# Performance work log

Measured on AMD Instinct MI355X. Metric: run time of the kernel, lower is better.

Reference implementation:

```python
import jax, jax.numpy as jnp
import numpy as np

N_NODES = 50000
N_EDGES = 800000
DIM = 128
HEADS = 4
NEG_SLOPE = 0.2
LN_EPS = 1e-5


def setup_inputs() -> dict:
    key = jax.random.key(0)
    ks = jax.random.split(key, 8)
    x = jax.random.normal(ks[0], (N_NODES, DIM), dtype=jnp.float32)
    edge_index = jax.random.randint(ks[1], (2, N_EDGES), 0, N_NODES, dtype=jnp.int32)
    W = jax.random.normal(ks[2], (DIM, DIM), dtype=jnp.float32) * (1.0 / np.sqrt(DIM))
    b = jnp.zeros((DIM,), dtype=jnp.float32)
    C = DIM // HEADS
    att_src = jax.random.normal(ks[3], (HEADS, C), dtype=jnp.float32) * 0.1
    att_dst = jax.random.normal(ks[4], (HEADS, C), dtype=jnp.float32) * 0.1
    ln_gamma = jnp.ones((DIM,), dtype=jnp.float32)
    ln_beta = jnp.zeros((DIM,), dtype=jnp.float32)
    prelu_w = jnp.full((1,), 0.25, dtype=jnp.float32)
    return {"x": x, "edge_index": edge_index, "W": W, "b": b,
            "att_src": att_src, "att_dst": att_dst,
            "ln_gamma": ln_gamma, "ln_beta": ln_beta, "prelu_w": prelu_w}


def reference(x, edge_index, W, b, att_src, att_dst, ln_gamma, ln_beta, prelu_w):
    N, D = x.shape
    H = HEADS
    C = D // H
    # shared linear transform (PyG GATConv lin_src == lin_dst for homogeneous input)
    xw = (x @ W).reshape(N, H, C)                      # [N,H,C]
    a_src = jnp.einsum('nhc,hc->nh', xw, att_src)      # [N,H]
    a_dst = jnp.einsum('nhc,hc->nh', xw, att_dst)      # [N,H]
    # add self loops (PyG default add_self_loops=True)
    loop = jnp.arange(N, dtype=edge_index.dtype)
    src = jnp.concatenate([edge_index[0], loop])       # [E+N]
    dst = jnp.concatenate([edge_index[1], loop])       # [E+N]
    # per-edge attention logits + segment softmax over destination
    alpha = jax.nn.leaky_relu(a_src[src] + a_dst[dst], NEG_SLOPE)   # [E+N,H]
    amax = jax.ops.segment_max(alpha, dst, num_segments=N)          # [N,H]
    alpha = jnp.exp(alpha - amax[dst])
    denom = jax.ops.segment_sum(alpha, dst, num_segments=N)         # [N,H]
    alpha = alpha / denom[dst]
    # weighted aggregation of source features
    msg = xw[src] * alpha[:, :, None]                               # [E+N,H,C]
    out = jax.ops.segment_sum(msg, dst, num_segments=N).reshape(N, D) + b
    # residual + LayerNorm + PReLU
    h = x + out
    mu = jnp.mean(h, axis=-1, keepdims=True)
    var = jnp.mean(jnp.square(h - mu), axis=-1, keepdims=True)
    h = (h - mu) * jax.lax.rsqrt(var + LN_EPS) * ln_gamma + ln_beta
    return jnp.where(h > 0, h, prelu_w[0] * h)
```

## Files before the change

### kernel.cpp

```cpp
#include <hip/hip_runtime.h>

#define NNODES 50000
#define NEDGES 800000
#define NEDGE4 200000
#define DIMF 128
#define NHEADS 4
#define NEG_SLOPE 0.2f
#define LN_EPS 1e-5f
#define SLOTS 64
#define NPERX 6250
#define NLB 782
#define SCB 2048

typedef int   v4i   __attribute__((ext_vector_type(4)));
typedef float v2f   __attribute__((ext_vector_type(2)));
typedef float v4f   __attribute__((ext_vector_type(4)));
typedef unsigned int v2u __attribute__((ext_vector_type(2)));
typedef short bf16x8 __attribute__((ext_vector_type(8)));
typedef float f32x4  __attribute__((ext_vector_type(4)));
typedef unsigned short u16x8 __attribute__((ext_vector_type(8)));

__device__ __forceinline__ unsigned short f2bf(float f) {
    unsigned int u = __float_as_uint(f);
    u = (u + 0x7fffu + ((u >> 16) & 1u)) >> 16;
    return (unsigned short)u;
}
__device__ __forceinline__ float bf2f(unsigned short u) {
    return __uint_as_float(((unsigned int)u) << 16);
}

__global__ __launch_bounds__(256) void k_prep(const float* __restrict__ W,
                                              unsigned short* __restrict__ WtG,
                                              int* __restrict__ cursor)
{
    const int idx = blockIdx.x * 256 + threadIdx.x;
    if (idx < DIMF * DIMF) {
        const int k = idx >> 7, col = idx & 127;
        WtG[col * 136 + k] = f2bf(W[idx]);
    }
    if (idx < NNODES) cursor[idx] = 0;
}

__global__ __launch_bounds__(256) void k_main(
    const float* __restrict__ x, const unsigned short* __restrict__ WtG,
    const float* __restrict__ att_src, const float* __restrict__ att_dst,
    unsigned char* __restrict__ xwb,
    float* __restrict__ asrc, float* __restrict__ adst,
    const int* __restrict__ esrc, const int* __restrict__ edst,
    int* __restrict__ cursor, unsigned short* __restrict__ perm)
{
    __shared__ unsigned short WtL[64 * 136];
    __shared__ float sAttS[128], sAttD[128];
    const int tid = threadIdx.x;

    if (blockIdx.x < SCB) {
        const int lo = (blockIdx.x & 7) * NPERX, hi = lo + NPERX;
        const v4i* es4 = (const v4i*)esrc;
        const v4i* ed4 = (const v4i*)edst;
        const int stride = (SCB >> 3) * 256;
        for (int e = (blockIdx.x >> 3) * 256 + tid; e < NEDGE4; e += stride) {
            v4i d4 = __builtin_nontemporal_load(ed4 + e);
            v4i s4 = __builtin_nontemporal_load(es4 + e);
            #pragma unroll
            for (int c = 0; c < 4; ++c) {
                const int dd = d4[c], ss = s4[c];
                if (dd >= lo && dd < hi) {
                    int p = atomicAdd(&cursor[dd], 1);
                    if (p < SLOTS) perm[(size_t)dd * SLOTS + p] = (unsigned short)ss;
                }
            }
        }
        return;
    }

    const int base = (blockIdx.x - SCB) * 64;

    if (tid < 128) sAttS[tid] = att_src[tid];
    else           sAttD[tid - 128] = att_dst[tid - 128];

    const int wv_   = tid >> 6;
    const int lane  = tid & 63;
    const int row16 = lane & 15;
    const int kg    = lane >> 4;
    const int grow_a = base + wv_ * 16 + row16;
    const int arow   = (grow_a < NNODES) ? grow_a : 0;

    bf16x8 af[4];
    #pragma unroll
    for (int ks = 0; ks < 4; ++ks) {
        const v4f* xr = (const v4f*)(x + (size_t)arow * DIMF + ks * 32 + kg * 8);
        const v4f xa = __builtin_nontemporal_load(xr);
        const v4f xb = __builtin_nontemporal_load(xr + 1);
        af[ks][0] = (short)f2bf(xa.x); af[ks][1] = (short)f2bf(xa.y);
        af[ks][2] = (short)f2bf(xa.z); af[ks][3] = (short)f2bf(xa.w);
        af[ks][4] = (short)f2bf(xb.x); af[ks][5] = (short)f2bf(xb.y);
        af[ks][6] = (short)f2bf(xb.z); af[ks][7] = (short)f2bf(xb.w);
    }

    f32x4 acc[8];
    #pragma unroll
    for (int ct = 0; ct < 8; ++ct) acc[ct] = (f32x4){0.f, 0.f, 0.f, 0.f};

    const uint4* g = (const uint4*)WtG;
    for (int hf = 0; hf < 2; ++hf) {
        __syncthreads();
        for (int i = tid; i < 1088; i += 256)
            ((uint4*)WtL)[i] = g[hf * 1088 + i];
        __syncthreads();
        #pragma unroll
        for (int ks = 0; ks < 4; ++ks) {
            #pragma unroll
            for (int ct = 0; ct < 4; ++ct) {
                const bf16x8 bfr = *(const bf16x8*)&WtL[(ct * 16 + row16) * 136 + ks * 32 + kg * 8];
                acc[hf * 4 + ct] = __builtin_amdgcn_mfma_f32_16x16x32_bf16(af[ks], bfr, acc[hf * 4 + ct], 0, 0, 0);
            }
        }
    }

    __syncthreads();
    unsigned short* OutL = WtL;
    #pragma unroll
    for (int ct = 0; ct < 8; ++ct) {
        #pragma unroll
        for (int r = 0; r < 4; ++r)
            OutL[(wv_ * 16 + kg * 4 + r) * 136 + ct * 16 + row16] = f2bf(acc[ct][r]);
    }
    __syncthreads();

    const int rowD = tid >> 2, seg = tid & 3;
    const int growD = base + rowD;
    if (growD < NNODES) {
        float ps = 0.f, pd = 0.f;
        #pragma unroll
        for (int q = 0; q < 4; ++q) {
            const u16x8 v = *(const u16x8*)&OutL[rowD * 136 + seg * 32 + q * 8];
            #pragma unroll
            for (int j = 0; j < 8; ++j) {
                const float f = bf2f(v[j]);
                const int c = seg * 32 + q * 8 + j;
                ps += f * sAttS[c];
                pd += f * sAttD[c];
            }
        }
        asrc[growD * NHEADS + seg] = ps;
        adst[growD * NHEADS + seg] = pd;
    }

    #pragma unroll
    for (int it = 0; it < 4; ++it) {
        const int f = tid + it * 256;
        const int row = f >> 4;
        const int c8  = (f & 15) * 8;
        if (base + row < NNODES) {
            const u16x8 v = *(const u16x8*)&OutL[row * 136 + c8];
            unsigned int lo, hi;
            lo = __builtin_amdgcn_cvt_pk_fp8_f32(bf2f(v[0]), bf2f(v[1]), 0, false);
            lo = __builtin_amdgcn_cvt_pk_fp8_f32(bf2f(v[2]), bf2f(v[3]), lo, true);
            hi = __builtin_amdgcn_cvt_pk_fp8_f32(bf2f(v[4]), bf2f(v[5]), 0, false);
            hi = __builtin_amdgcn_cvt_pk_fp8_f32(bf2f(v[6]), bf2f(v[7]), hi, true);
            v2u pk; pk.x = lo; pk.y = hi;
            __builtin_nontemporal_store(pk, (v2u*)(xwb + (size_t)(base + row) * DIMF + c8));
        }
    }
}

__global__ __launch_bounds__(256) void k_weights(
    const float4* __restrict__ asrc4, const float4* __restrict__ adst4,
    const int* __restrict__ cursor, const unsigned short* __restrict__ perm,
    ushort4* __restrict__ wperm)
{
    const int wid  = (blockIdx.x * 256 + threadIdx.x) >> 6;
    const int lane = threadIdx.x & 63;
    if (wid >= NNODES) return;

    int cnt = cursor[wid];
    if (cnt > SLOTS) cnt = SLOTS;
    const int cnt2 = (cnt + 15) & ~15;
    const float4 dv = adst4[wid];

    ushort4 wu = make_ushort4(0, 0, 0, 0);
    if (lane < cnt) {
        const int s = (int)perm[(size_t)wid * SLOTS + lane];
        const float4 ae = asrc4[s];
        float l0 = ae.x + dv.x, l1 = ae.y + dv.y;
        float l2 = ae.z + dv.z, l3 = ae.w + dv.w;
        l0 = (l0 > 0.f) ? l0 : NEG_SLOPE * l0;
        l1 = (l1 > 0.f) ? l1 : NEG_SLOPE * l1;
        l2 = (l2 > 0.f) ? l2 : NEG_SLOPE * l2;
        l3 = (l3 > 0.f) ? l3 : NEG_SLOPE * l3;
        wu.x = f2bf(__expf(l0)); wu.y = f2bf(__expf(l1));
        wu.z = f2bf(__expf(l2)); wu.w = f2bf(__expf(l3));
    }
    if (lane < cnt2) wperm[(size_t)wid * SLOTS + lane] = wu;
}

__global__ __launch_bounds__(256) void k_gat(
    const float* __restrict__ x, const float* __restrict__ bias,
    const float* __restrict__ asrc, const float* __restrict__ adst,
    const unsigned short* __restrict__ xwb16,
    const int* __restrict__ cursor, const unsigned short* __restrict__ perm,
    const unsigned short* __restrict__ wperm_u16,
    const float* __restrict__ ln_g, const float* __restrict__ ln_b,
    const float* __restrict__ prelu_w, float* __restrict__ out)
{
    const int wid  = (blockIdx.x * 256 + threadIdx.x) >> 6;
    const int lane = threadIdx.x & 63;
    if (wid >= NNODES) return;
    const int myh = lane >> 4;
    const int hb  = lane & 3;

    const float adh_b = adst[wid * NHEADS + hb];
    float lgS = asrc[wid * NHEADS + hb] + adh_b;
    lgS = (lgS > 0.f) ? lgS : NEG_SLOPE * lgS;
    const float wself_b = __expf(lgS);

    int cnt = cursor[wid];
    if (cnt > SLOTS) cnt = SLOTS;
    const int sidx = (lane < cnt) ? (int)perm[(size_t)wid * SLOTS + lane] : 0;

    const float wself = __shfl(wself_b, myh);
    const v2f pself = __builtin_amdgcn_cvt_pk_f32_fp8(
        (unsigned int)xwb16[(size_t)wid * 64 + lane], false);
    float acc0 = wself * pself.x;
    float acc1 = wself * pself.y;
    float dsum = 0.f;

    const int jmax = (cnt + 15) >> 4;
    for (int j = 0; j < jmax; ++j) {
        const unsigned short wu = wperm_u16[(size_t)wid * 256 + j * 64 + lane];
        const float wv = __uint_as_float(((unsigned)wu) << 16);
        dsum += wv;

        #pragma unroll
        for (int b = 0; b < 2; ++b) {
            const int ebase = j * 16 + b * 8;
            int s_[8]; float w_[8]; unsigned short v_[8];
            #pragma unroll
            for (int e = 0; e < 8; ++e) {
                s_[e] = __shfl(sidx, ebase + e);
                w_[e] = __shfl(wv, ((b * 8 + e) << 2) | myh);
            }
            #pragma unroll
            for (int e = 0; e < 8; ++e)
                v_[e] = xwb16[(size_t)s_[e] * 64 + lane];
            #pragma unroll
            for (int e = 0; e < 8; ++e) {
                const v2f p = __builtin_amdgcn_cvt_pk_f32_fp8((unsigned int)v_[e], false);
                acc0 += w_[e] * p.x;
                acc1 += w_[e] * p.y;
            }
        }
    }

    #pragma unroll
    for (int o = 4; o < 64; o <<= 1) dsum += __shfl_xor(dsum, o);
    const float wsum = __shfl(dsum + wself_b, myh);

    const float inv = 1.0f / wsum;
    const int c = lane * 2;
    const float2 xr = ((const float2*)x)[(size_t)wid * 64 + lane];
    float h0 = xr.x + acc0 * inv + bias[c];
    float h1 = xr.y + acc1 * inv + bias[c + 1];

    float s1 = h0 + h1, s2 = h0 * h0 + h1 * h1;
    #pragma unroll
    for (int o = 1; o < 64; o <<= 1) {
        s1 += __shfl_xor(s1, o);
        s2 += __shfl_xor(s2, o);
    }
    const float mu  = s1 * (1.f / 128.f);
    const float var = s2 * (1.f / 128.f) - mu * mu;
    const float r   = rsqrtf(var + LN_EPS);

    float g0 = (h0 - mu) * r * ln_g[c]     + ln_b[c];
    float g1 = (h1 - mu) * r * ln_g[c + 1] + ln_b[c + 1];
    const float pw = prelu_w[0];
    g0 = (g0 > 0.f) ? g0 : pw * g0;
    g1 = (g1 > 0.f) ? g1 : pw * g1;

    v2f gv; gv.x = g0; gv.y = g1;
    __builtin_nontemporal_store(gv, (v2f*)out + (size_t)wid * 64 + lane);
}

extern "C" void kernel_launch(void* const* d_in, const int* in_sizes, int n_in,
                              void* d_out, int out_size, void* d_ws, size_t ws_size,
                              hipStream_t stream)
{
    const float* x    = (const float*)d_in[0];
    const int*   eidx = (const int*)  d_in[1];
    const float* W    = (const float*)d_in[2];
    const float* bias = (const float*)d_in[3];
    const float* attS = (const float*)d_in[4];
    const float* attD = (const float*)d_in[5];
    const float* lng  = (const float*)d_in[6];
    const float* lnb  = (const float*)d_in[7];
    const float* pre  = (const float*)d_in[8];

    const int* esrc = eidx;
    const int* edst = eidx + NEDGES;

    unsigned char* xwb = (unsigned char*)d_ws;
    float* asrc    = (float*)(xwb + (size_t)NNODES * DIMF);
    float* adst    = asrc + (size_t)NNODES * NHEADS;
    int*   cursor  = (int*)(adst + (size_t)NNODES * NHEADS);
    unsigned short* perm = (unsigned short*)(cursor + NNODES);
    ushort4* wperm = (ushort4*)(perm + (size_t)NNODES * SLOTS);
    unsigned short* WtG = (unsigned short*)(wperm + (size_t)NNODES * SLOTS);

    k_prep<<<dim3(196), dim3(256), 0, stream>>>(W, WtG, cursor);

    k_main<<<dim3(SCB + NLB), dim3(256), 0, stream>>>(
        x, WtG, attS, attD, xwb, asrc, adst, esrc, edst, cursor, perm);

    k_weights<<<dim3((NNODES * 64 + 255) / 256), dim3(256), 0, stream>>>(
        (const float4*)asrc, (const float4*)adst, cursor, perm, wperm);

    k_gat<<<dim3((NNODES * 64 + 255) / 256), dim3(256), 0, stream>>>(
        x, bias, asrc, adst, (const unsigned short*)xwb, cursor, perm,
        (const unsigned short*)wperm, lng, lnb, pre, (float*)d_out);
}
```

Measured before the change: 107.4 us.

## Fuse attention weight computation into aggregation kernel and pack edge indices

Removes the separate k_weights kernel. Each wave now computes its node's per-edge exp attention weights directly and stages them in shared memory, which avoids a global write and re-read of the weight array and one launch. k_prep also packs the src/dst indices of every edge into one 32-bit word, so each of the 8 bucketing passes in k_main reads half as many bytes. In exchange the prep kernel grows to cover all edges and adds a full edge-list pass, and the packing assumes node ids fit in 16 bits.

```diff
diff --git a/kernel.cpp b/kernel.cpp
--- a/kernel.cpp
+++ b/kernel.cpp
@@ -13,6 +13,7 @@
 #define SCB 2048
 
 typedef int   v4i   __attribute__((ext_vector_type(4)));
+typedef unsigned int v4u __attribute__((ext_vector_type(4)));
 typedef float v2f   __attribute__((ext_vector_type(2)));
 typedef float v4f   __attribute__((ext_vector_type(4)));
 typedef unsigned int v2u __attribute__((ext_vector_type(2)));
@@ -29,9 +30,10 @@
     return __uint_as_float(((unsigned int)u) << 16);
 }
 
-__global__ __launch_bounds__(256) void k_prep(const float* __restrict__ W,
-                                              unsigned short* __restrict__ WtG,
-                                              int* __restrict__ cursor)
+__global__ __launch_bounds__(256) void k_prep(
+    const float* __restrict__ W, const int* __restrict__ esrc,
+    const int* __restrict__ edst, unsigned short* __restrict__ WtG,
+    int* __restrict__ cursor, unsigned int* __restrict__ epack)
 {
     const int idx = blockIdx.x * 256 + threadIdx.x;
     if (idx < DIMF * DIMF) {
@@ -39,6 +41,8 @@
         WtG[col * 136 + k] = f2bf(W[idx]);
     }
     if (idx < NNODES) cursor[idx] = 0;
+    if (idx < NEDGES)
+        epack[idx] = ((unsigned int)edst[idx] << 16) | (unsigned int)esrc[idx];
 }
 
 __global__ __launch_bounds__(256) void k_main(
@@ -46,7 +50,7 @@
     const float* __restrict__ att_src, const float* __restrict__ att_dst,
     unsigned char* __restrict__ xwb,
     float* __restrict__ asrc, float* __restrict__ adst,
-    const int* __restrict__ esrc, const int* __restrict__ edst,
+    const unsigned int* __restrict__ epack,
     int* __restrict__ cursor, unsigned short* __restrict__ perm)
 {
     __shared__ unsigned short WtL[64 * 136];
@@ -54,19 +58,18 @@
     const int tid = threadIdx.x;
 
     if (blockIdx.x < SCB) {
-        const int lo = (blockIdx.x & 7) * NPERX, hi = lo + NPERX;
-        const v4i* es4 = (const v4i*)esrc;
-        const v4i* ed4 = (const v4i*)edst;
+        const unsigned int lo = (blockIdx.x & 7) * NPERX, hi = lo + NPERX;
+        const v4u* ep4 = (const v4u*)epack;
         const int stride = (SCB >> 3) * 256;
         for (int e = (blockIdx.x >> 3) * 256 + tid; e < NEDGE4; e += stride) {
-            v4i d4 = __builtin_nontemporal_load(ed4 + e);
-            v4i s4 = __builtin_nontemporal_load(es4 + e);
+            v4u p4 = __builtin_nontemporal_load(ep4 + e);
             #pragma unroll
             for (int c = 0; c < 4; ++c) {
-                const int dd = d4[c], ss = s4[c];
+                const unsigned int dd = p4[c] >> 16;
                 if (dd >= lo && dd < hi) {
                     int p = atomicAdd(&cursor[dd], 1);
-                    if (p < SLOTS) perm[(size_t)dd * SLOTS + p] = (unsigned short)ss;
+                    if (p < SLOTS)
+                        perm[(size_t)dd * SLOTS + p] = (unsigned short)(p4[c] & 0xffffu);
                 }
             }
         }
@@ -164,59 +167,49 @@
     }
 }
 
-__global__ __launch_bounds__(256) void k_weights(
-    const float4* __restrict__ asrc4, const float4* __restrict__ adst4,
-    const int* __restrict__ cursor, const unsigned short* __restrict__ perm,
-    ushort4* __restrict__ wperm)
-{
-    const int wid  = (blockIdx.x * 256 + threadIdx.x) >> 6;
-    const int lane = threadIdx.x & 63;
-    if (wid >= NNODES) return;
-
-    int cnt = cursor[wid];
-    if (cnt > SLOTS) cnt = SLOTS;
-    const int cnt2 = (cnt + 15) & ~15;
-    const float4 dv = adst4[wid];
-
-    ushort4 wu = make_ushort4(0, 0, 0, 0);
-    if (lane < cnt) {
-        const int s = (int)perm[(size_t)wid * SLOTS + lane];
-        const float4 ae = asrc4[s];
-        float l0 = ae.x + dv.x, l1 = ae.y + dv.y;
-        float l2 = ae.z + dv.z, l3 = ae.w + dv.w;
-        l0 = (l0 > 0.f) ? l0 : NEG_SLOPE * l0;
-        l1 = (l1 > 0.f) ? l1 : NEG_SLOPE * l1;
-        l2 = (l2 > 0.f) ? l2 : NEG_SLOPE * l2;
-        l3 = (l3 > 0.f) ? l3 : NEG_SLOPE * l3;
-        wu.x = f2bf(__expf(l0)); wu.y = f2bf(__expf(l1));
-        wu.z = f2bf(__expf(l2)); wu.w = f2bf(__expf(l3));
-    }
-    if (lane < cnt2) wperm[(size_t)wid * SLOTS + lane] = wu;
-}
-
 __global__ __launch_bounds__(256) void k_gat(
     const float* __restrict__ x, const float* __restrict__ bias,
-    const float* __restrict__ asrc, const float* __restrict__ adst,
+    const float4* __restrict__ asrc4, const float4* __restrict__ adst4,
     const unsigned short* __restrict__ xwb16,
     const int* __restrict__ cursor, const unsigned short* __restrict__ perm,
-    const unsigned short* __restrict__ wperm_u16,
     const float* __restrict__ ln_g, const float* __restrict__ ln_b,
     const float* __restrict__ prelu_w, float* __restrict__ out)
 {
+    __shared__ unsigned short wlds[4][256];
     const int wid  = (blockIdx.x * 256 + threadIdx.x) >> 6;
     const int lane = threadIdx.x & 63;
+    const int wv4  = threadIdx.x >> 6;
     if (wid >= NNODES) return;
     const int myh = lane >> 4;
     const int hb  = lane & 3;
 
-    const float adh_b = adst[wid * NHEADS + hb];
-    float lgS = asrc[wid * NHEADS + hb] + adh_b;
-    lgS = (lgS > 0.f) ? lgS : NEG_SLOPE * lgS;
-    const float wself_b = __expf(lgS);
-
     int cnt = cursor[wid];
     if (cnt > SLOTS) cnt = SLOTS;
     const int sidx = (lane < cnt) ? (int)perm[(size_t)wid * SLOTS + lane] : 0;
+
+    const float4 dv = adst4[wid];
+    {
+        ushort4 wu = make_ushort4(0, 0, 0, 0);
+        if (lane < cnt) {
+            const float4 ae = asrc4[sidx];
+            float l0 = ae.x + dv.x, l1 = ae.y + dv.y;
+            float l2 = ae.z + dv.z, l3 = ae.w + dv.w;
+            l0 = (l0 > 0.f) ? l0 : NEG_SLOPE * l0;
+            l1 = (l1 > 0.f) ? l1 : NEG_SLOPE * l1;
+            l2 = (l2 > 0.f) ? l2 : NEG_SLOPE * l2;
+            l3 = (l3 > 0.f) ? l3 : NEG_SLOPE * l3;
+            wu.x = f2bf(__expf(l0)); wu.y = f2bf(__expf(l1));
+            wu.z = f2bf(__expf(l2)); wu.w = f2bf(__expf(l3));
+        }
+        *(ushort4*)&wlds[wv4][lane * 4] = wu;
+    }
+
+    const float ad_hb = (hb == 0) ? dv.x : (hb == 1) ? dv.y : (hb == 2) ? dv.z : dv.w;
+    const float4 avw = asrc4[wid];
+    const float as_hb = (hb == 0) ? avw.x : (hb == 1) ? avw.y : (hb == 2) ? avw.z : avw.w;
+    float lgS = as_hb + ad_hb;
+    lgS = (lgS > 0.f) ? lgS : NEG_SLOPE * lgS;
+    const float wself_b = __expf(lgS);
 
     const float wself = __shfl(wself_b, myh);
     const v2f pself = __builtin_amdgcn_cvt_pk_f32_fp8(
@@ -227,7 +220,7 @@
 
     const int jmax = (cnt + 15) >> 4;
     for (int j = 0; j < jmax; ++j) {
-        const unsigned short wu = wperm_u16[(size_t)wid * 256 + j * 64 + lane];
+        const unsigned short wu = wlds[wv4][j * 64 + lane];
         const float wv = __uint_as_float(((unsigned)wu) << 16);
         dsum += wv;
 
@@ -304,18 +297,16 @@
     float* adst    = asrc + (size_t)NNODES * NHEADS;
     int*   cursor  = (int*)(adst + (size_t)NNODES * NHEADS);
     unsigned short* perm = (unsigned short*)(cursor + NNODES);
-    ushort4* wperm = (ushort4*)(perm + (size_t)NNODES * SLOTS);
-    unsigned short* WtG = (unsigned short*)(wperm + (size_t)NNODES * SLOTS);
-
-    k_prep<<<dim3(196), dim3(256), 0, stream>>>(W, WtG, cursor);
+    unsigned int* epack = (unsigned int*)(perm + (size_t)NNODES * SLOTS);
+    unsigned short* WtG = (unsigned short*)(epack + NEDGES);
+
+    k_prep<<<dim3((NEDGES + 255) / 256), dim3(256), 0, stream>>>(
+        W, esrc, edst, WtG, cursor, epack);
 
     k_main<<<dim3(SCB + NLB), dim3(256), 0, stream>>>(
-        x, WtG, attS, attD, xwb, asrc, adst, esrc, edst, cursor, perm);
-
-    k_weights<<<dim3((NNODES * 64 + 255) / 256), dim3(256), 0, stream>>>(
-        (const float4*)asrc, (const float4*)adst, cursor, perm, wperm);
+        x, WtG, attS, attD, xwb, asrc, adst, epack, cursor, perm);
 
     k_gat<<<dim3((NNODES * 64 + 255) / 256), dim3(256), 0, stream>>>(
-        x, bias, asrc, adst, (const unsigned short*)xwb, cursor, perm,
-        (const unsigned short*)wperm, lng, lnb, pre, (float*)d_out);
-}
+        x, bias, (const float4*)asrc, (const float4*)adst,
+        (const unsigned short*)xwb, cursor, perm, lng, lnb, pre, (float*)d_out);
+}
```

Result: faster. 102.2 us (-4.9%).
